# Kernel tuning notes

Hardware: AMD Instinct MI355X
Metric: run time of the kernel (lower is better)

The kernel has to match this reference:

```python
import jax, jax.numpy as jnp
import numpy as np

N = 100000
MAX_HOPS = 3
EPS = 1e-16


def _gat_conv(x, src, dst, W, a_src, a_dst, bias, heads, out_c, concat):
    """PyG-style GATConv (eval mode, self-loops, negative_slope=0.2)."""
    n = x.shape[0]
    loop = jnp.arange(n, dtype=src.dtype)
    s = jnp.concatenate([src, loop])
    d = jnp.concatenate([dst, loop])
    h = (x @ W).reshape(n, heads, out_c)                      # [N,H,C]
    al_s = (h * a_src).sum(-1)                                # [N,H]
    al_d = (h * a_dst).sum(-1)                                # [N,H]
    e = jax.nn.leaky_relu(al_s[s] + al_d[d], 0.2)             # [E,H]
    e_max = jax.ops.segment_max(e, d, num_segments=n)
    e = jnp.exp(e - e_max[d])
    denom = jax.ops.segment_sum(e, d, num_segments=n)
    alpha = e / (denom[d] + EPS)                              # edge softmax per dst
    out = jax.ops.segment_sum(h[s] * alpha[:, :, None], d, num_segments=n)  # [N,H,C]
    out = out.reshape(n, heads * out_c) if concat else out.mean(axis=1)
    return out + bias


def _hierarchy(src, dst, seed, n, max_hops):
    """BFS hop distance from seeds; one-hot rows, all-zero if unreached."""
    reached = seed
    dist = jnp.where(seed, 0, max_hops + 1)
    for h in range(1, max_hops + 1):
        msg = jax.ops.segment_max(reached[src].astype(jnp.int32), dst, num_segments=n)
        nbr = msg > 0
        dist = jnp.where(nbr & (~reached), h, dist)
        reached = reached | nbr
    mask = (dist[:, None] == jnp.arange(max_hops + 1)[None, :]).astype(jnp.float32)
    hop_counts = jnp.argmax(mask, axis=1).astype(jnp.float32)  # all-zero row -> 0, like torch
    return mask, hop_counts


def setup_inputs() -> dict:
    key = jax.random.key(0)
    ks = jax.random.split(key, 20)
    in_aug = 128 + MAX_HOPS + 1  # 132
    out_channels = 40
    g = lambda k, shp: (jax.random.normal(k, shp, dtype=jnp.float32) * 0.1)
    return {
        "x": jax.random.normal(ks[0], (N, 128), dtype=jnp.float32),
        "edge_index": jax.random.randint(ks[1], (2, 1600000), 0, N, dtype=jnp.int64),
        "seed_mask": jax.random.randint(ks[2], (N,), 0, 100, dtype=jnp.int32),
        "W1": g(ks[3], (in_aug, 8 * 8)), "a1s": g(ks[4], (8, 8)), "a1d": g(ks[5], (8, 8)), "b1": jnp.zeros((64,), jnp.float32),
        "W2": g(ks[6], (64, 8 * 16)), "a2s": g(ks[7], (8, 16)), "a2d": g(ks[8], (8, 16)), "b2": jnp.zeros((128,), jnp.float32),
        "W3": g(ks[9], (128, out_channels)), "a3s": g(ks[10], (1, out_channels)), "a3d": g(ks[11], (1, out_channels)), "b3": jnp.zeros((out_channels,), jnp.float32),
        "Wg": g(ks[12], (129, 1)), "bg": jnp.zeros((1,), jnp.float32),
    }


def reference(x, edge_index, seed_mask, W1, a1s, a1d, b1, W2, a2s, a2d, b2,
              W3, a3s, a3d, b3, Wg, bg):
    src, dst = edge_index[0], edge_index[1]
    seed = seed_mask == 0
    hmask, hop_counts = _hierarchy(src, dst, seed, N, MAX_HOPS)
    aug = jnp.concatenate([x, hmask], axis=1)
    h1 = jax.nn.elu(_gat_conv(aug, src, dst, W1, a1s, a1d, b1, 8, 8, True))
    h2 = _gat_conv(h1, src, dst, W2, a2s, a2d, b2, 8, 16, True)
    gate_in = jnp.concatenate([h2, hop_counts[:, None]], axis=1)
    gate = jax.nn.sigmoid(gate_in @ Wg + bg)
    h2 = h2 * gate
    h3 = _gat_conv(h2, src, dst, W3, a3s, a3d, b3, 1, 40, False)
    return jax.nn.log_softmax(h3, axis=1)
```

## Files before the change

### kernel.cpp

```cpp
#include <hip/hip_runtime.h>
#include <hip/hip_bf16.h>
#include <hip/hip_fp16.h>
#include <math.h>

#define MAXH 3
#define NSB 9
#define NS (1 << NSB)
#define SRCBITS 17
#define SRCMASK ((1 << SRCBITS) - 1)
#define LOG2E 1.4426950408889634f
typedef unsigned int u32;
typedef unsigned char u8;
typedef unsigned short u16;

using bf16x8 = __attribute__((ext_vector_type(8))) short;
using f32x4  = __attribute__((ext_vector_type(4))) float;

__device__ __forceinline__ float fexp2(float x) {
#if __has_builtin(__builtin_amdgcn_exp2f)
    return __builtin_amdgcn_exp2f(x);
#else
    return exp2f(x);
#endif
}
__device__ __forceinline__ u16 f2bf(float f) {
    u32 u = __float_as_uint(f);
    u32 r = ((u >> 16) & 1u) + 0x7fffu;
    return (u16)((u + r) >> 16);
}

__global__ void k_bfs_init(const int* __restrict__ seed_mask, int* dist, int n) {
    int i = blockIdx.x * blockDim.x + threadIdx.x;
    if (i < n) dist[i] = (seed_mask[i] == 0) ? 0 : (MAXH + 1);
}
__global__ void k_rbits_init(const int* __restrict__ seed_mask, u32* rbits, int nw, int n) {
    int w = blockIdx.x * blockDim.x + threadIdx.x;
    if (w < nw) {
        u32 b = 0;
        int base = w * 32;
        int lim = min(32, n - base);
        for (int j = 0; j < lim; j++)
            if (seed_mask[base + j] == 0) b |= (1u << j);
        rbits[w] = b;
    }
}
__global__ void k_bfs_scan(const int* __restrict__ rowptr, const int* __restrict__ csr_src,
                           const u32* __restrict__ rbits, u8* __restrict__ nbr, int n) {
    int i = blockIdx.x * blockDim.x + threadIdx.x;
    if (i < n) {
        if (!((rbits[i >> 5] >> (i & 31)) & 1u)) {
            int beg = rowptr[i], end = rowptr[i + 1];
            u8 f = 0;
            for (int k = beg; k < end; k++) {
                int s = csr_src[k];
                if ((rbits[s >> 5] >> (s & 31)) & 1u) { f = 1; break; }
            }
            nbr[i] = f;
        }
    }
}
__global__ void k_bfs_node(u32* rbits, int* dist, const u8* __restrict__ nbr, int h, int n) {
    int i = blockIdx.x * blockDim.x + threadIdx.x;
    if (i < n) {
        if (nbr[i] && !((rbits[i >> 5] >> (i & 31)) & 1u)) {
            dist[i] = h;
            atomicOr(&rbits[i >> 5], 1u << (i & 31));
        }
    }
}

__global__ void k_bincount(const int4* __restrict__ dst4, int* bincnt, int E4) {
    __shared__ int cnt[256];
    int t = threadIdx.x;
    cnt[t] = 0;
    __syncthreads();
    int i = blockIdx.x * 256 + t;
    if (i < E4) {
        int4 d = dst4[i];
        atomicAdd(&cnt[d.x >> NSB], 1);
        atomicAdd(&cnt[d.y >> NSB], 1);
        atomicAdd(&cnt[d.z >> NSB], 1);
        atomicAdd(&cnt[d.w >> NSB], 1);
    }
    __syncthreads();
    if (cnt[t] > 0) atomicAdd(&bincnt[t], cnt[t]);
}

__global__ void k_binscan(const int* __restrict__ bincnt, int* binbase, int* bincur,
                          int* rowptr, int BINS, int E, int n) {
    __shared__ int sd[256];
    int t = threadIdx.x;
    int v = (t < BINS) ? bincnt[t] : 0;
    sd[t] = v;
    __syncthreads();
    for (int off = 1; off < 256; off <<= 1) {
        int add = (t >= off) ? sd[t - off] : 0;
        __syncthreads();
        sd[t] += add;
        __syncthreads();
    }
    int excl = sd[t] - v;
    if (t < BINS) { binbase[t] = excl; bincur[t] = excl; }
    if (t == 0) { binbase[BINS] = E; rowptr[n] = E; }
}

__global__ void k_binscatter(const int4* __restrict__ src4, const int4* __restrict__ dst4,
                             int* bincur, int* __restrict__ pairs, int E4, int BINS) {
    __shared__ int cnt[256], base[256];
    int t = threadIdx.x;
    cnt[t] = 0;
    __syncthreads();
    int i = blockIdx.x * 256 + t;
    int bin[4], rank[4], pack[4];
    bool valid = i < E4;
    if (valid) {
        int4 s = src4[i], d = dst4[i];
        bin[0] = d.x >> NSB; pack[0] = ((d.x & (NS - 1)) << SRCBITS) | s.x;
        bin[1] = d.y >> NSB; pack[1] = ((d.y & (NS - 1)) << SRCBITS) | s.y;
        bin[2] = d.z >> NSB; pack[2] = ((d.z & (NS - 1)) << SRCBITS) | s.z;
        bin[3] = d.w >> NSB; pack[3] = ((d.w & (NS - 1)) << SRCBITS) | s.w;
        rank[0] = atomicAdd(&cnt[bin[0]], 1);
        rank[1] = atomicAdd(&cnt[bin[1]], 1);
        rank[2] = atomicAdd(&cnt[bin[2]], 1);
        rank[3] = atomicAdd(&cnt[bin[3]], 1);
    }
    __syncthreads();
    if (t < BINS && cnt[t] > 0) base[t] = atomicAdd(&bincur[t], cnt[t]);
    __syncthreads();
    if (valid) {
        pairs[base[bin[0]] + rank[0]] = pack[0];
        pairs[base[bin[1]] + rank[1]] = pack[1];
        pairs[base[bin[2]] + rank[2]] = pack[2];
        pairs[base[bin[3]] + rank[3]] = pack[3];
    }
}

__global__ void k_binsort(const int* __restrict__ pairs, const int* __restrict__ binbase,
                          int* __restrict__ rowptr, int* __restrict__ csr_src, int n) {
    __shared__ int hist[NS];
    const int b = blockIdx.x, t = threadIdx.x;
    const int nbeg = b << NSB;
    const int ebeg = binbase[b];
    const int ecnt = binbase[b + 1] - ebeg;
    hist[t] = 0; hist[t + 256] = 0;
    __syncthreads();
    for (int i = t; i < ecnt; i += 256)
        atomicAdd(&hist[(u32)pairs[ebeg + i] >> SRCBITS], 1);
    for (int d = 1; d < NS; d <<= 1) {
        __syncthreads();
        int idx = (t + 1) * (d << 1) - 1;
        if (idx < NS) hist[idx] += hist[idx - d];
    }
    __syncthreads();
    if (t == 0) hist[NS - 1] = 0;
    for (int d = NS / 2; d >= 1; d >>= 1) {
        __syncthreads();
        int idx = (t + 1) * (d << 1) - 1;
        if (idx < NS) { int tmp = hist[idx - d]; hist[idx - d] = hist[idx]; hist[idx] += tmp; }
    }
    __syncthreads();
    int g0 = nbeg + t, g1 = nbeg + t + 256;
    if (g0 < n) rowptr[g0] = ebeg + hist[t];
    if (g1 < n) rowptr[g1] = ebeg + hist[t + 256];
    __syncthreads();
    for (int i = t; i < ecnt; i += 256) {
        int p = pairs[ebeg + i];
        int pos = atomicAdd(&hist[(u32)p >> SRCBITS], 1);
        csr_src[ebeg + pos] = p & SRCMASK;
    }
}

template <int SK, int MBW>
__launch_bounds__(256)
__global__ void k_gemm_mfma1(const float* __restrict__ A, const float* __restrict__ W,
                             const float* __restrict__ a_s, const float* __restrict__ a_d,
                             const int* __restrict__ dist, __half* __restrict__ out,
                             float* __restrict__ als, float* __restrict__ ald, int n) {
    constexpr int K = 128, NREAL = 64, NTT = 5, AH = 8, C = 8;
    constexpr int KT = K / 32;
    constexpr int NTCOL = (NTT - 1) * 16;
    __shared__ u16 WT[NTT * 16 * SK];
    __shared__ u16 sAW[4][16 * SK];
    __shared__ float sAug[4][64];
    __shared__ float sAugA[4][16];

    for (int idx = threadIdx.x; idx < NTT * 16 * K; idx += 256) {
        int c = idx / K, k = idx % K;
        float v;
        if (c < NREAL) {
            v = W[k * NREAL + c];
        } else {
            int j = (c - NTCOL) & 7;
            const float* aw = (c < NTCOL + AH) ? a_s : a_d;
            float accv = 0.0f;
            for (int cc = 0; cc < C; cc++) accv += W[k * NREAL + j * C + cc] * aw[j * C + cc];
            v = accv * LOG2E;
        }
        WT[c * SK + k] = f2bf(v);
    }
    {
        int t = threadIdx.x;
        int d = t >> 6, c = t & 63;
        sAug[d][c] = W[(K + d) * NREAL + c];
        if (t < 64) {
            int dd = t >> 4, j = t & 15;
            int hh = j & 7;
            const float* aw = (j < 8) ? a_s : a_d;
            float accv = 0.0f;
            for (int cc = 0; cc < C; cc++)
                accv += W[(K + dd) * NREAL + hh * C + cc] * aw[hh * C + cc];
            sAugA[dd][j] = accv * LOG2E;
        }
    }
    __syncthreads();

    const int lane = threadIdx.x & 63;
    const int l15 = lane & 15;
    const int kg = lane >> 4;
    const int w = threadIdx.x >> 6;
    const int wid = blockIdx.x * 4 + w;

    bf16x8 bfr[NTT][KT];
#pragma unroll
    for (int nt = 0; nt < NTT; nt++)
#pragma unroll
        for (int kt = 0; kt < KT; kt++)
            bfr[nt][kt] = *(const bf16x8*)&WT[(nt * 16 + l15) * SK + kt * 32 + kg * 8];

    for (int mb = 0; mb < MBW; mb++) {
        const int rowbase = (wid * MBW + mb) * 16;
        if (rowbase >= n) break;
        {
            int r = lane >> 2, c4b = lane & 3;
            const float* xr = A + (size_t)(rowbase + r) * K;
#pragma unroll
            for (int j = 0; j < 8; j++) {
                int c4 = c4b + j * 4;
                float4 v = *(const float4*)&xr[c4 * 4];
                ushort4 o;
                o.x = f2bf(v.x); o.y = f2bf(v.y); o.z = f2bf(v.z); o.w = f2bf(v.w);
                *(ushort4*)&sAW[w][r * SK + c4 * 4] = o;
            }
        }
        bf16x8 af[KT];
#pragma unroll
        for (int kt = 0; kt < KT; kt++)
            af[kt] = *(const bf16x8*)&sAW[w][l15 * SK + kt * 32 + kg * 8];
        f32x4 acc[NTT];
#pragma unroll
        for (int nt = 0; nt < NTT; nt++) acc[nt] = f32x4{0.f, 0.f, 0.f, 0.f};
#pragma unroll
        for (int kt = 0; kt < KT; kt++)
#pragma unroll
            for (int nt = 0; nt < NTT; nt++)
                acc[nt] = __builtin_amdgcn_mfma_f32_16x16x32_bf16(af[kt], bfr[nt][kt],
                                                                  acc[nt], 0, 0, 0);
        int rows[4], dd[4];
#pragma unroll
        for (int r = 0; r < 4; r++) {
            rows[r] = rowbase + kg * 4 + r;
            dd[r] = dist[rows[r]];
        }
#pragma unroll
        for (int nt = 0; nt < NTT - 1; nt++) {
            int c = nt * 16 + l15;
#pragma unroll
            for (int r = 0; r < 4; r++) {
                float v = acc[nt][r];
                if (dd[r] <= MAXH) v += sAug[dd[r]][c];
                out[(size_t)rows[r] * NREAL + c] = __float2half(v);
            }
        }
#pragma unroll
        for (int r = 0; r < 4; r++) {
            float v = acc[NTT - 1][r];
            if (dd[r] <= MAXH) v += sAugA[dd[r]][l15];
            if (l15 < AH) als[(size_t)rows[r] * AH + l15] = v;
            else ald[(size_t)rows[r] * AH + (l15 - AH)] = v;
        }
    }
}

template <int K, int NREAL, int NTT, int AH, int C, int SK, int MBW>
__launch_bounds__(256)
__global__ void k_gemm_mfma(const u16* __restrict__ A, const float* __restrict__ W,
                            const float* __restrict__ a_s, const float* __restrict__ a_d,
                            __half* __restrict__ out, float* __restrict__ als,
                            float* __restrict__ ald, int n) {
    constexpr int KT = K / 32;
    constexpr int NTCOL = (NTT - 1) * 16;
    __shared__ u16 WT[NTT * 16 * SK];
    for (int idx = threadIdx.x; idx < NTT * 16 * K; idx += 256) {
        int c = idx / K, k = idx % K;
        float v = 0.0f;
        if (c < NREAL) {
            v = W[k * NREAL + c];
        } else if (c >= NTCOL && c < NTCOL + 2 * AH) {
            int j = (c - NTCOL) % AH;
            const float* aw = (c < NTCOL + AH) ? a_s : a_d;
            float accv = 0.0f;
            for (int cc = 0; cc < C; cc++) accv += W[k * NREAL + j * C + cc] * aw[j * C + cc];
            v = accv * LOG2E;
        }
        WT[c * SK + k] = f2bf(v);
    }
    __syncthreads();

    const int lane = threadIdx.x & 63;
    const int l15 = lane & 15;
    const int kg = lane >> 4;
    const int wid = blockIdx.x * 4 + (threadIdx.x >> 6);

    bf16x8 bfr[NTT][KT];
#pragma unroll
    for (int nt = 0; nt < NTT; nt++)
#pragma unroll
        for (int kt = 0; kt < KT; kt++)
            bfr[nt][kt] = *(const bf16x8*)&WT[(nt * 16 + l15) * SK + kt * 32 + kg * 8];

    for (int mb = 0; mb < MBW; mb++) {
        const int rowbase = (wid * MBW + mb) * 16;
        if (rowbase >= n) break;
        bf16x8 af[KT];
#pragma unroll
        for (int kt = 0; kt < KT; kt++)
            af[kt] = *(const bf16x8*)&A[(size_t)(rowbase + l15) * K + kt * 32 + kg * 8];
        f32x4 acc[NTT];
#pragma unroll
        for (int nt = 0; nt < NTT; nt++) acc[nt] = f32x4{0.f, 0.f, 0.f, 0.f};
#pragma unroll
        for (int kt = 0; kt < KT; kt++)
#pragma unroll
            for (int nt = 0; nt < NTT; nt++)
                acc[nt] = __builtin_amdgcn_mfma_f32_16x16x32_bf16(af[kt], bfr[nt][kt],
                                                                  acc[nt], 0, 0, 0);
#pragma unroll
        for (int nt = 0; nt < NTT - 1; nt++) {
            int c = nt * 16 + l15;
            if (c < NREAL) {
#pragma unroll
                for (int r = 0; r < 4; r++) {
                    int row = rowbase + kg * 4 + r;
                    out[(size_t)row * NREAL + c] = __float2half(acc[nt][r]);
                }
            }
        }
#pragma unroll
        for (int r = 0; r < 4; r++) {
            int row = rowbase + kg * 4 + r;
            float v = acc[NTT - 1][r];
            if (l15 < AH) als[(size_t)row * AH + l15] = v;
            else if (l15 < 2 * AH) ald[(size_t)row * AH + (l15 - AH)] = v;
        }
    }
}

template <int H, int C, int CH, int MODE, typename OT>
__launch_bounds__(256)
__global__ void k_gat(const int* __restrict__ rowptr, const int* __restrict__ csr_src,
                      const __half* __restrict__ h, const float* __restrict__ als,
                      const float* __restrict__ ald, const float* __restrict__ bias,
                      const int* __restrict__ dist, const float* __restrict__ Wg,
                      const float* __restrict__ bg, OT* __restrict__ out, int n) {
    constexpr int TOT = H * C;
    constexpr int NL = TOT / CH;
    const int lane = threadIdx.x & 63;
    const int node = blockIdx.x * 4 + (threadIdx.x >> 6);
    if (node >= n) return;
    const int beg = rowptr[node];
    const int deg = rowptr[node + 1] - beg;

    const int cl = (lane < NL) ? lane : 0;
    const int hd = (cl * CH) / C;
    const float ald_hd = ald[(size_t)node * H + hd];
    const float t0 = als[(size_t)node * H + hd] + ald_hd;
    const float m0 = fmaxf(t0, 0.2f * t0);
    const float c0 = ald_hd - m0;
    const float c1 = 0.2f * ald_hd - m0;

    float s = 1.0f;
    float ax = 0.0f, ay = 0.0f;
    __half2 acc2;
    if (MODE == 2) {
        acc2 = *(const __half2*)(h + (size_t)node * TOT + cl * 2);
    } else {
        ax = __half2float(h[(size_t)node * TOT + cl]);
    }

    auto body = [&](int sN) {
        float a = als[(size_t)sN * H + hd];
        float v = fmaxf(a + c0, fmaf(a, 0.2f, c1));
        float p = fexp2(v);
        s += p;
        if (MODE == 2) {
            __half2 ph = __float2half2_rn(p);
            acc2 = __hfma2(ph, *(const __half2*)(h + (size_t)sN * TOT + cl * 2), acc2);
        } else {
            ax += p * __half2float(h[(size_t)sN * TOT + cl]);
        }
    };

    for (int base = 0; base < deg; base += 64) {
        const int myE = base + lane;
        int sReg = (myE < deg) ? csr_src[beg + myE] : 0;
        const int cnt = min(64, deg - base);
        int e = 0;
        for (; e + 4 <= cnt; e += 4) {
            body(__builtin_amdgcn_readlane(sReg, e));
            body(__builtin_amdgcn_readlane(sReg, e + 1));
            body(__builtin_amdgcn_readlane(sReg, e + 2));
            body(__builtin_amdgcn_readlane(sReg, e + 3));
        }
        for (; e < cnt; e++) body(__builtin_amdgcn_readlane(sReg, e));
    }

    const float inv = 1.0f / (s + 1e-16f);
    if (MODE == 2) {
        float2 av = __half22float2(acc2);
        ax = av.x; ay = av.y;
    }
    float vx = ax * inv + bias[cl * CH];
    float vy = (CH == 2) ? (ay * inv + bias[cl * CH + 1]) : 0.0f;

    if (MODE == 1) {
        vx = vx > 0.0f ? vx : expm1f(vx);
        ((u16*)out)[(size_t)node * TOT + cl] = f2bf(vx);
    } else if (MODE == 2) {
        float2 wg = *(const float2*)&Wg[cl * 2];
        float part = vx * wg.x + vy * wg.y;
#pragma unroll
        for (int off = 32; off > 0; off >>= 1) part += __shfl_xor(part, off);
        int d = dist[node];
        float hop = (d <= MAXH) ? (float)d : 0.0f;
        float g = 1.0f / (1.0f + __expf(-(part + hop * Wg[128] + bg[0])));
        ushort2 wv;
        wv.x = f2bf(vx * g);
        wv.y = f2bf(vy * g);
        *(ushort2*)&((u16*)out)[(size_t)node * TOT + cl * 2] = wv;
    } else if (MODE == 3) {
        float v = (lane < NL) ? vx : -INFINITY;
        float mm = v;
#pragma unroll
        for (int off = 32; off > 0; off >>= 1) mm = fmaxf(mm, __shfl_xor(mm, off));
        float ex = (lane < NL) ? __expf(v - mm) : 0.0f;
        float ss = ex;
#pragma unroll
        for (int off = 32; off > 0; off >>= 1) ss += __shfl_xor(ss, off);
        float ls = logf(ss);
        if (lane < NL) ((float*)out)[(size_t)node * TOT + cl] = v - mm - ls;
    }
}

static inline int nblk(long long t, int b) { return (int)((t + b - 1) / b); }

extern "C" void kernel_launch(void* const* d_in, const int* in_sizes, int n_in,
                              void* d_out, int out_size, void* d_ws, size_t ws_size,
                              hipStream_t stream) {
    const float* x = (const float*)d_in[0];
    const int* eidx = (const int*)d_in[1];
    const int* seed_mask = (const int*)d_in[2];
    const float* W1 = (const float*)d_in[3];
    const float* a1s = (const float*)d_in[4];
    const float* a1d = (const float*)d_in[5];
    const float* b1 = (const float*)d_in[6];
    const float* W2 = (const float*)d_in[7];
    const float* a2s = (const float*)d_in[8];
    const float* a2d = (const float*)d_in[9];
    const float* b2 = (const float*)d_in[10];
    const float* W3 = (const float*)d_in[11];
    const float* a3s = (const float*)d_in[12];
    const float* a3d = (const float*)d_in[13];
    const float* b3 = (const float*)d_in[14];
    const float* Wg = (const float*)d_in[15];
    const float* bg = (const float*)d_in[16];

    const int n = in_sizes[0] / 128;
    const long long E = in_sizes[1] / 2;
    const int E4 = (int)(E / 4);
    const int4* src4 = (const int4*)eidx;
    const int4* dst4 = (const int4*)(eidx + E);
    const int BINS = (n + NS - 1) >> NSB;
    const int NW = (n + 31) / 32;

    char* ws = (char*)d_ws;
    size_t off = 0;
    auto alloc = [&](size_t bytes) -> void* {
        void* p = ws + off;
        off = (off + bytes + 255) & ~(size_t)255;
        return p;
    };
    int* dist    = (int*)alloc((size_t)n * 4);
    u32* rbits   = (u32*)alloc((size_t)NW * 4);
    u8* nbr      = (u8*)alloc((size_t)n);
    int* rowptr  = (int*)alloc((size_t)(n + 1) * 4);
    int* bincnt  = (int*)alloc(256 * 4);
    int* binbase = (int*)alloc(257 * 4);
    int* bincur  = (int*)alloc(256 * 4);
    int* csr_src = (int*)alloc((size_t)E * 4);
    float* als   = (float*)alloc((size_t)n * 8 * 4);
    float* ald   = (float*)alloc((size_t)n * 8 * 4);
    __half* hbuf = (__half*)alloc((size_t)n * 128 * 2);
    u16* abuf    = (u16*)alloc((size_t)n * 128 * 2);
    int* pairs   = (int*)abuf;
    float* out = (float*)d_out;

    const int BS = 256;

    hipMemsetAsync(bincnt, 0, 256 * 4, stream);
    k_bfs_init<<<nblk(n, BS), BS, 0, stream>>>(seed_mask, dist, n);
    k_rbits_init<<<nblk(NW, BS), BS, 0, stream>>>(seed_mask, rbits, NW, n);
    k_bincount<<<nblk(E4, BS), BS, 0, stream>>>(dst4, bincnt, E4);
    k_binscan<<<1, 256, 0, stream>>>(bincnt, binbase, bincur, rowptr, BINS, (int)E, n);
    k_binscatter<<<nblk(E4, BS), BS, 0, stream>>>(src4, dst4, bincur, pairs, E4, BINS);
    k_binsort<<<BINS, 256, 0, stream>>>(pairs, binbase, rowptr, csr_src, n);

    for (int h = 1; h <= MAXH; h++) {
        k_bfs_scan<<<nblk(n, BS), BS, 0, stream>>>(rowptr, csr_src, rbits, nbr, n);
        k_bfs_node<<<nblk(n, BS), BS, 0, stream>>>(rbits, dist, nbr, h, n);
    }

    const int mblocks = (n + 15) / 16;
    const int gmf = (mblocks + 15) / 16;

    k_gemm_mfma1<136, 4>
        <<<gmf, 256, 0, stream>>>(x, W1, a1s, a1d, dist, hbuf, als, ald, n);
    k_gat<8, 8, 1, 1, u16><<<nblk(n, 4), 256, 0, stream>>>(
        rowptr, csr_src, hbuf, als, ald, b1, nullptr, nullptr, nullptr, abuf, n);

    k_gemm_mfma<64, 128, 9, 8, 16, 72, 4>
        <<<gmf, 256, 0, stream>>>(abuf, W2, a2s, a2d, hbuf, als, ald, n);
    k_gat<8, 16, 2, 2, u16><<<nblk(n, 4), 256, 0, stream>>>(
        rowptr, csr_src, hbuf, als, ald, b2, dist, Wg, bg, abuf, n);

    k_gemm_mfma<128, 40, 4, 1, 40, 136, 4>
        <<<gmf, 256, 0, stream>>>(abuf, W3, a3s, a3d, hbuf, als, ald, n);
    k_gat<1, 40, 1, 3, float><<<nblk(n, 4), 256, 0, stream>>>(
        rowptr, csr_src, hbuf, als, ald, b3, nullptr, nullptr, nullptr, out, n);
}
```

Before: 438.2 us.

## Fuse BFS init and steps with ballot bitmasks, shrink sort bins, enlarge GAT blocks

Init, rbits building and the bincnt memset are merged into one kernel that builds 64-bit reached masks with wave ballots. Each BFS hop becomes a single kernel that reads the old mask and writes a new one (ping-pong), replacing the scan-plus-node pair and its atomics, which cuts launches. The CSR bin size drops from 512 to 256 nodes, giving up to 512 bins with larger shared arrays in the bin kernels. The GAT kernels now run 1024-thread blocks covering 16 nodes each instead of 4, which may change occupancy.

```diff
diff --git a/kernel.cpp b/kernel.cpp
--- a/kernel.cpp
+++ b/kernel.cpp
@@ -4,12 +4,13 @@
 #include <math.h>
 
 #define MAXH 3
-#define NSB 9
+#define NSB 8
 #define NS (1 << NSB)
 #define SRCBITS 17
 #define SRCMASK ((1 << SRCBITS) - 1)
 #define LOG2E 1.4426950408889634f
 typedef unsigned int u32;
+typedef unsigned long long u64;
 typedef unsigned char u8;
 typedef unsigned short u16;
 
@@ -29,50 +30,44 @@
     return (u16)((u + r) >> 16);
 }
 
-__global__ void k_bfs_init(const int* __restrict__ seed_mask, int* dist, int n) {
-    int i = blockIdx.x * blockDim.x + threadIdx.x;
-    if (i < n) dist[i] = (seed_mask[i] == 0) ? 0 : (MAXH + 1);
-}
-__global__ void k_rbits_init(const int* __restrict__ seed_mask, u32* rbits, int nw, int n) {
-    int w = blockIdx.x * blockDim.x + threadIdx.x;
-    if (w < nw) {
-        u32 b = 0;
-        int base = w * 32;
-        int lim = min(32, n - base);
-        for (int j = 0; j < lim; j++)
-            if (seed_mask[base + j] == 0) b |= (1u << j);
-        rbits[w] = b;
-    }
-}
-__global__ void k_bfs_scan(const int* __restrict__ rowptr, const int* __restrict__ csr_src,
-                           const u32* __restrict__ rbits, u8* __restrict__ nbr, int n) {
-    int i = blockIdx.x * blockDim.x + threadIdx.x;
+__global__ void k_init(const int* __restrict__ seed_mask, int* dist, u64* rb64,
+                       int* bincnt, int n) {
+    int i = blockIdx.x * 256 + threadIdx.x;
+    int lane = threadIdx.x & 63;
+    bool seed = (i < n) && (seed_mask[i] == 0);
+    if (i < n) dist[i] = seed ? 0 : (MAXH + 1);
+    u64 b = __ballot(seed);
+    if (lane == 0 && (i & ~63) < n) rb64[i >> 6] = b;
+    if (blockIdx.x == 0) {
+        bincnt[threadIdx.x] = 0;
+        bincnt[threadIdx.x + 256] = 0;
+    }
+}
+
+__global__ void k_bfs_step(const int* __restrict__ rowptr, const int* __restrict__ csr_src,
+                           const u32* __restrict__ rbOld, u64* rbNew, int* dist,
+                           int h, int n) {
+    int i = blockIdx.x * 256 + threadIdx.x;
+    int lane = threadIdx.x & 63;
+    bool reached = false;
     if (i < n) {
-        if (!((rbits[i >> 5] >> (i & 31)) & 1u)) {
+        reached = (rbOld[i >> 5] >> (i & 31)) & 1u;
+        if (!reached) {
             int beg = rowptr[i], end = rowptr[i + 1];
-            u8 f = 0;
             for (int k = beg; k < end; k++) {
                 int s = csr_src[k];
-                if ((rbits[s >> 5] >> (s & 31)) & 1u) { f = 1; break; }
+                if ((rbOld[s >> 5] >> (s & 31)) & 1u) { reached = true; dist[i] = h; break; }
             }
-            nbr[i] = f;
-        }
-    }
-}
-__global__ void k_bfs_node(u32* rbits, int* dist, const u8* __restrict__ nbr, int h, int n) {
-    int i = blockIdx.x * blockDim.x + threadIdx.x;
-    if (i < n) {
-        if (nbr[i] && !((rbits[i >> 5] >> (i & 31)) & 1u)) {
-            dist[i] = h;
-            atomicOr(&rbits[i >> 5], 1u << (i & 31));
-        }
-    }
+        }
+    }
+    u64 b = __ballot(reached);
+    if (lane == 0 && (i & ~63) < n) rbNew[i >> 6] = b;
 }
 
 __global__ void k_bincount(const int4* __restrict__ dst4, int* bincnt, int E4) {
-    __shared__ int cnt[256];
+    __shared__ int cnt[512];
     int t = threadIdx.x;
-    cnt[t] = 0;
+    cnt[t] = 0; cnt[t + 256] = 0;
     __syncthreads();
     int i = blockIdx.x * 256 + t;
     if (i < E4) {
@@ -84,16 +79,17 @@
     }
     __syncthreads();
     if (cnt[t] > 0) atomicAdd(&bincnt[t], cnt[t]);
+    if (cnt[t + 256] > 0) atomicAdd(&bincnt[t + 256], cnt[t + 256]);
 }
 
 __global__ void k_binscan(const int* __restrict__ bincnt, int* binbase, int* bincur,
                           int* rowptr, int BINS, int E, int n) {
-    __shared__ int sd[256];
+    __shared__ int sd[512];
     int t = threadIdx.x;
     int v = (t < BINS) ? bincnt[t] : 0;
     sd[t] = v;
     __syncthreads();
-    for (int off = 1; off < 256; off <<= 1) {
+    for (int off = 1; off < 512; off <<= 1) {
         int add = (t >= off) ? sd[t - off] : 0;
         __syncthreads();
         sd[t] += add;
@@ -106,9 +102,9 @@
 
 __global__ void k_binscatter(const int4* __restrict__ src4, const int4* __restrict__ dst4,
                              int* bincur, int* __restrict__ pairs, int E4, int BINS) {
-    __shared__ int cnt[256], base[256];
+    __shared__ int cnt[512], base[512];
     int t = threadIdx.x;
-    cnt[t] = 0;
+    cnt[t] = 0; cnt[t + 256] = 0;
     __syncthreads();
     int i = blockIdx.x * 256 + t;
     int bin[4], rank[4], pack[4];
@@ -125,7 +121,8 @@
         rank[3] = atomicAdd(&cnt[bin[3]], 1);
     }
     __syncthreads();
-    if (t < BINS && cnt[t] > 0) base[t] = atomicAdd(&bincur[t], cnt[t]);
+    if (cnt[t] > 0) base[t] = atomicAdd(&bincur[t], cnt[t]);
+    if (cnt[t + 256] > 0) base[t + 256] = atomicAdd(&bincur[t + 256], cnt[t + 256]);
     __syncthreads();
     if (valid) {
         pairs[base[bin[0]] + rank[0]] = pack[0];
@@ -142,7 +139,7 @@
     const int nbeg = b << NSB;
     const int ebeg = binbase[b];
     const int ecnt = binbase[b + 1] - ebeg;
-    hist[t] = 0; hist[t + 256] = 0;
+    hist[t] = 0;
     __syncthreads();
     for (int i = t; i < ecnt; i += 256)
         atomicAdd(&hist[(u32)pairs[ebeg + i] >> SRCBITS], 1);
@@ -159,9 +156,8 @@
         if (idx < NS) { int tmp = hist[idx - d]; hist[idx - d] = hist[idx]; hist[idx] += tmp; }
     }
     __syncthreads();
-    int g0 = nbeg + t, g1 = nbeg + t + 256;
+    int g0 = nbeg + t;
     if (g0 < n) rowptr[g0] = ebeg + hist[t];
-    if (g1 < n) rowptr[g1] = ebeg + hist[t + 256];
     __syncthreads();
     for (int i = t; i < ecnt; i += 256) {
         int p = pairs[ebeg + i];
@@ -356,7 +352,7 @@
 }
 
 template <int H, int C, int CH, int MODE, typename OT>
-__launch_bounds__(256)
+__launch_bounds__(1024)
 __global__ void k_gat(const int* __restrict__ rowptr, const int* __restrict__ csr_src,
                       const __half* __restrict__ h, const float* __restrict__ als,
                       const float* __restrict__ ald, const float* __restrict__ bias,
@@ -365,7 +361,7 @@
     constexpr int TOT = H * C;
     constexpr int NL = TOT / CH;
     const int lane = threadIdx.x & 63;
-    const int node = blockIdx.x * 4 + (threadIdx.x >> 6);
+    const int node = blockIdx.x * 16 + (threadIdx.x >> 6);
     if (node >= n) return;
     const int beg = rowptr[node];
     const int deg = rowptr[node + 1] - beg;
@@ -480,7 +476,7 @@
     const int4* src4 = (const int4*)eidx;
     const int4* dst4 = (const int4*)(eidx + E);
     const int BINS = (n + NS - 1) >> NSB;
-    const int NW = (n + 31) / 32;
+    const int NW64 = (n + 63) / 64;
 
     char* ws = (char*)d_ws;
     size_t off = 0;
@@ -490,12 +486,12 @@
         return p;
     };
     int* dist    = (int*)alloc((size_t)n * 4);
-    u32* rbits   = (u32*)alloc((size_t)NW * 4);
-    u8* nbr      = (u8*)alloc((size_t)n);
+    u64* rbA     = (u64*)alloc((size_t)NW64 * 8);
+    u64* rbB     = (u64*)alloc((size_t)NW64 * 8);
     int* rowptr  = (int*)alloc((size_t)(n + 1) * 4);
-    int* bincnt  = (int*)alloc(256 * 4);
-    int* binbase = (int*)alloc(257 * 4);
-    int* bincur  = (int*)alloc(256 * 4);
+    int* bincnt  = (int*)alloc(512 * 4);
+    int* binbase = (int*)alloc(513 * 4);
+    int* bincur  = (int*)alloc(512 * 4);
     int* csr_src = (int*)alloc((size_t)E * 4);
     float* als   = (float*)alloc((size_t)n * 8 * 4);
     float* ald   = (float*)alloc((size_t)n * 8 * 4);
@@ -506,34 +502,35 @@
 
     const int BS = 256;
 
-    hipMemsetAsync(bincnt, 0, 256 * 4, stream);
-    k_bfs_init<<<nblk(n, BS), BS, 0, stream>>>(seed_mask, dist, n);
-    k_rbits_init<<<nblk(NW, BS), BS, 0, stream>>>(seed_mask, rbits, NW, n);
+    k_init<<<nblk(n, BS), BS, 0, stream>>>(seed_mask, dist, rbA, bincnt, n);
+
     k_bincount<<<nblk(E4, BS), BS, 0, stream>>>(dst4, bincnt, E4);
-    k_binscan<<<1, 256, 0, stream>>>(bincnt, binbase, bincur, rowptr, BINS, (int)E, n);
+    k_binscan<<<1, 512, 0, stream>>>(bincnt, binbase, bincur, rowptr, BINS, (int)E, n);
     k_binscatter<<<nblk(E4, BS), BS, 0, stream>>>(src4, dst4, bincur, pairs, E4, BINS);
     k_binsort<<<BINS, 256, 0, stream>>>(pairs, binbase, rowptr, csr_src, n);
 
-    for (int h = 1; h <= MAXH; h++) {
-        k_bfs_scan<<<nblk(n, BS), BS, 0, stream>>>(rowptr, csr_src, rbits, nbr, n);
-        k_bfs_node<<<nblk(n, BS), BS, 0, stream>>>(rbits, dist, nbr, h, n);
-    }
+    k_bfs_step<<<nblk(n, BS), BS, 0, stream>>>(rowptr, csr_src, (const u32*)rbA, rbB,
+                                               dist, 1, n);
+    k_bfs_step<<<nblk(n, BS), BS, 0, stream>>>(rowptr, csr_src, (const u32*)rbB, rbA,
+                                               dist, 2, n);
+    k_bfs_step<<<nblk(n, BS), BS, 0, stream>>>(rowptr, csr_src, (const u32*)rbA, rbB,
+                                               dist, 3, n);
 
     const int mblocks = (n + 15) / 16;
     const int gmf = (mblocks + 15) / 16;
 
     k_gemm_mfma1<136, 4>
         <<<gmf, 256, 0, stream>>>(x, W1, a1s, a1d, dist, hbuf, als, ald, n);
-    k_gat<8, 8, 1, 1, u16><<<nblk(n, 4), 256, 0, stream>>>(
+    k_gat<8, 8, 1, 1, u16><<<nblk(n, 16), 1024, 0, stream>>>(
         rowptr, csr_src, hbuf, als, ald, b1, nullptr, nullptr, nullptr, abuf, n);
 
     k_gemm_mfma<64, 128, 9, 8, 16, 72, 4>
         <<<gmf, 256, 0, stream>>>(abuf, W2, a2s, a2d, hbuf, als, ald, n);
-    k_gat<8, 16, 2, 2, u16><<<nblk(n, 4), 256, 0, stream>>>(
+    k_gat<8, 16, 2, 2, u16><<<nblk(n, 16), 1024, 0, stream>>>(
         rowptr, csr_src, hbuf, als, ald, b2, dist, Wg, bg, abuf, n);
 
     k_gemm_mfma<128, 40, 4, 1, 40, 136, 4>
         <<<gmf, 256, 0, stream>>>(abuf, W3, a3s, a3d, hbuf, als, ald, n);
-    k_gat<1, 40, 1, 3, float><<<nblk(n, 4), 256, 0, stream>>>(
+    k_gat<1, 40, 1, 3, float><<<nblk(n, 16), 1024, 0, stream>>>(
         rowptr, csr_src, hbuf, als, ald, b3, nullptr, nullptr, nullptr, out, n);
 }
```

Result: no change. 441.5 us (+0.8%).
